# Optimization experiments

Hardware: AMD Instinct MI355X
Metric: run time of the kernel (lower is better)

The kernel has to match this reference:

```python
import jax, jax.numpy as jnp
import numpy as np

TEMPERATURE = 0.07
LOG_EPS = 1e-20
MEAN_EPS = 1e-6


def setup_inputs() -> dict:
    key = jax.random.key(0)
    k1, k2, k3 = jax.random.split(key, 3)
    B, T1, I1, C = 64, 33, 197, 512  # 1+seqlen=33, 1+14*14=197
    text_embeds = jax.random.normal(k1, (B, T1, C), dtype=jnp.float32)
    video_embeds = jax.random.normal(k2, (B, I1, C), dtype=jnp.float32)
    text_attn_mask = jax.random.randint(k3, (B, T1), 0, 2).astype(jnp.int32)
    # guarantee every row has at least one attended (non-CLS) token
    text_attn_mask = text_attn_mask.at[:, :2].set(1)
    return {"text_embeds": text_embeds, "video_embeds": video_embeds,
            "text_attn_mask": text_attn_mask}


def reference(text_embeds, video_embeds, text_attn_mask):
    # NOTE: original normalizes over dim=1 (sequence axis), kept faithfully.
    te = text_embeds / jnp.linalg.norm(text_embeds, axis=1, keepdims=True)
    ve = video_embeds / jnp.linalg.norm(video_embeds, axis=1, keepdims=True)
    mask = text_attn_mask[:, 1:].astype(bool)          # [B, T] (trim CLS)
    text_latents = te[:, 1:, :]                        # [B, T, C]
    # full late-interaction score tensor, scaled (multiplied) by temperature
    sim = jnp.einsum('xtd,yid->xyti', text_latents, ve) * TEMPERATURE  # [X,Y,T,I]

    # text -> image: max over image tokens, masked mean over text tokens
    t2i = sim.max(axis=-1)                             # [X, Y, T]
    m = mask[None, :, None, :]                         # [1, B, 1, T] (X must == B)
    numer = jnp.where(m, t2i[None], 0.0).sum(axis=-1)  # [1, B, Y]
    denom = jnp.maximum(mask.sum(axis=-1).astype(sim.dtype), MEAN_EPS)[None, :, None]
    text_to_image = numer / denom                      # [1, B, Y]

    # image -> text: masked max over text tokens, mean over image tokens
    # (computed in the original module but unused in the returned loss)
    m5 = mask[None, :, None, :, None]                  # [1, B, 1, T, 1]
    neg = -jnp.finfo(sim.dtype).max
    image_to_text = jnp.where(m5, sim[None], neg).max(axis=-2).mean(axis=-1)  # [1,B,Y]
    del image_to_text  # dead in original: loss = text_to_image_loss only

    t2i_exp = jnp.exp(text_to_image)                   # [1, B, Y]
    pos = jnp.diagonal(t2i_exp, axis1=-2, axis2=-1)    # [1, min(B, Y)]
    den = t2i_exp.sum(axis=-1)                         # [1, B]
    loss = -jnp.log(pos / den + LOG_EPS).mean(axis=-1)  # [1]
    return loss
```

## Files before the change

### kernel.cpp

```cpp
#include <hip/hip_runtime.h>
#include <hip/hip_bf16.h>
#include <float.h>
#include <math.h>

#define BB 64
#define T1 33
#define TT 32
#define II 197
#define CC 512
#define TEMP 0.07f

typedef float f32x4 __attribute__((ext_vector_type(4)));
typedef int i32x4 __attribute__((ext_vector_type(4)));
typedef int i32x8 __attribute__((ext_vector_type(8)));

#define TL_OFF  0
#define VE_OFF  (1 << 20)
#define TTI_OFF ((1 << 20) + (8 << 20))
#define KS_STRIDE   32768
#define GRP_STRIDE  131072

__global__ __launch_bounds__(512) void norm_all_kernel(const float* __restrict__ text,
                                                       const float* __restrict__ video,
                                                       unsigned char* __restrict__ tl8,
                                                       unsigned char* __restrict__ ve8) {
  int b = blockIdx.x, hz = blockIdx.y, tid = threadIdx.x;
  bool isV = hz < 4;
  int h2 = isV ? hz : hz - 4;
  const float* src = isV ? (video + (size_t)b * II * CC) : (text + (size_t)b * T1 * CC);
  int n = isV ? II : T1;

  __shared__ float cache[II][132];
  __shared__ float red[16][128];
  __shared__ float rn[128];

  {
    int c4 = tid & 31, rg = tid >> 5;
    const float* p = src + h2 * 128 + c4 * 4;
    float4 s = {0.f, 0.f, 0.f, 0.f};
    for (int i = rg; i < n; i += 16) {
      float4 v = *(const float4*)(p + (size_t)i * CC);
      *(float4*)&cache[i][c4 * 4] = v;
      s.x += v.x * v.x; s.y += v.y * v.y; s.z += v.z * v.z; s.w += v.w * v.w;
    }
    *(float4*)&red[rg][c4 * 4] = s;
  }
  __syncthreads();
  if (tid < 128) {
    float s = 0.f;
#pragma unroll
    for (int g = 0; g < 16; ++g) s += red[g][tid];
    rn[tid] = 1.0f / sqrtf(s);
  }
  __syncthreads();

  if (isV) {
    for (int S = tid; S < 13 * 128; S += 512) {
      int fb = S >> 7, h = (S >> 6) & 1, lane = S & 63;
      int i = fb * 16 + (lane & 15);
      int kloc = ((lane >> 4) & 3) * 32 + h * 16;
      unsigned int wd[4];
#pragma unroll
      for (int q = 0; q < 4; ++q) {
        f32x4 u = {0.f, 0.f, 0.f, 0.f};
        if (i < II) u = *(const f32x4*)&cache[i][kloc + q * 4];
        f32x4 r = *(const f32x4*)&rn[kloc + q * 4];
        int wv = __builtin_amdgcn_cvt_pk_fp8_f32(u[0] * r[0], u[1] * r[1], 0, 0);
        wv = __builtin_amdgcn_cvt_pk_fp8_f32(u[2] * r[2], u[3] * r[3], wv, 1);
        wd[q] = (unsigned int)wv;
      }
      unsigned char* dst = ve8 + (size_t)b * GRP_STRIDE + h2 * KS_STRIDE +
                           fb * 2048 + h * 1024 + lane * 16;
      *(uint4*)dst = make_uint4(wd[0], wd[1], wd[2], wd[3]);
    }
  } else if (tid < 256) {
    int fa_local = tid >> 7, h = (tid >> 6) & 1, lane = tid & 63;
    int t = fa_local * 16 + (lane & 15);
    int kloc = ((lane >> 4) & 3) * 32 + h * 16;
    unsigned int wd[4];
#pragma unroll
    for (int q = 0; q < 4; ++q) {
      f32x4 u = *(const f32x4*)&cache[1 + t][kloc + q * 4];
      f32x4 r = *(const f32x4*)&rn[kloc + q * 4];
      int wv = __builtin_amdgcn_cvt_pk_fp8_f32(u[0] * r[0], u[1] * r[1], 0, 0);
      wv = __builtin_amdgcn_cvt_pk_fp8_f32(u[2] * r[2], u[3] * r[3], wv, 1);
      wd[q] = (unsigned int)wv;
    }
    int fa = (b & 7) * 2 + fa_local;
    unsigned char* dst = tl8 + (size_t)(b >> 3) * GRP_STRIDE + h2 * KS_STRIDE +
                         fa * 2048 + h * 1024 + lane * 16;
    *(uint4*)dst = make_uint4(wd[0], wd[1], wd[2], wd[3]);
  }
}

__global__ __launch_bounds__(512, 4) void sim_kernel(const unsigned char* __restrict__ tl8,
                                                     const unsigned char* __restrict__ ve8,
                                                     const int* __restrict__ mask,
                                                     float* __restrict__ tti) {
  int L = blockIdx.x;
  int xcd = L & 7;
  int idx = L >> 3;
  int y = xcd * 8 + (idx & 7);
  int xcb = idx >> 3;

  int tid = threadIdx.x;
  int w = tid >> 6, lane = tid & 63;
  int wm = w & 1;
  int wn = w >> 1;

  __shared__ float smax[4 * 64];

  const unsigned char* Abase =
      tl8 + (size_t)(xcb >> 2) * GRP_STRIDE + (size_t)(xcb & 3) * 4 * 2048;
  const unsigned char* Bbase = ve8 + (size_t)y * GRP_STRIDE;

  f32x4 acc[2][4] = {};

#pragma unroll 1
  for (int s = 0; s < 4; ++s) {
    const unsigned char* ab = Abase + (size_t)s * KS_STRIDE + lane * 16;
    const unsigned char* bb = Bbase + (size_t)s * KS_STRIDE + lane * 16;

    i32x8 aop[2];
#pragma unroll
    for (int ma = 0; ma < 2; ++ma) {
      const unsigned char* p = ab + (wm * 2 + ma) * 2048;
      i32x4 h0 = *(const i32x4*)p;
      i32x4 h1 = *(const i32x4*)(p + 1024);
      aop[ma] = __builtin_shufflevector(h0, h1, 0, 1, 2, 3, 4, 5, 6, 7);
    }

#pragma unroll
    for (int nb = 0; nb < 3; ++nb) {
      int fb = wn + 4 * nb;
      const unsigned char* p = bb + fb * 2048;
      i32x4 h0 = *(const i32x4*)p;
      i32x4 h1 = *(const i32x4*)(p + 1024);
      i32x8 bop = __builtin_shufflevector(h0, h1, 0, 1, 2, 3, 4, 5, 6, 7);
#pragma unroll
      for (int ma = 0; ma < 2; ++ma)
        acc[ma][nb] = __builtin_amdgcn_mfma_scale_f32_16x16x128_f8f6f4(
            aop[ma], bop, acc[ma][nb], 0, 0,
            0, 0x7F7F7F7F, 0, 0x7F7F7F7F);
    }
    if (wn == 0) {
      const unsigned char* p = bb + 12 * 2048;
      i32x4 h0 = *(const i32x4*)p;
      i32x4 h1 = *(const i32x4*)(p + 1024);
      i32x8 bop = __builtin_shufflevector(h0, h1, 0, 1, 2, 3, 4, 5, 6, 7);
#pragma unroll
      for (int ma = 0; ma < 2; ++ma)
        acc[ma][3] = __builtin_amdgcn_mfma_scale_f32_16x16x128_f8f6f4(
            aop[ma], bop, acc[ma][3], 0, 0,
            0, 0x7F7F7F7F, 0, 0x7F7F7F7F);
    }
  }

  int col = lane & 15, gq = lane >> 4;
  int nfrag = (wn == 0) ? 4 : 3;
  bool valid[4];
#pragma unroll
  for (int nb = 0; nb < 4; ++nb) {
    int fb = wn + 4 * nb;
    valid[nb] = (nb < nfrag) && (fb * 16 + col < II);
  }

  float mx[2][4];
#pragma unroll
  for (int ma = 0; ma < 2; ++ma)
#pragma unroll
    for (int reg = 0; reg < 4; ++reg) {
      float m = -FLT_MAX;
#pragma unroll
      for (int nb = 0; nb < 4; ++nb)
        if (valid[nb]) m = fmaxf(m, acc[ma][nb][reg]);
      mx[ma][reg] = m;
    }
#pragma unroll
  for (int st = 1; st <= 8; st <<= 1)
#pragma unroll
    for (int ma = 0; ma < 2; ++ma)
#pragma unroll
      for (int reg = 0; reg < 4; ++reg)
        mx[ma][reg] = fmaxf(mx[ma][reg], __shfl_xor(mx[ma][reg], st));

  if (col == 0) {
#pragma unroll
    for (int ma = 0; ma < 2; ++ma)
#pragma unroll
      for (int reg = 0; reg < 4; ++reg)
        smax[wn * 64 + wm * 32 + ma * 16 + gq * 4 + reg] = mx[ma][reg];
  }
  __syncthreads();

  if (tid < 64) {
    int r = tid;
    float m = fmaxf(fmaxf(smax[r], smax[64 + r]),
                    fmaxf(smax[128 + r], smax[192 + r]));
    int x = xcb * 2 + (r >> 5), tt = r & 31;
    int mk = mask[x * T1 + 1 + tt];
    float num = mk ? m * TEMP : 0.f;
    float cnt = mk ? 1.f : 0.f;
#pragma unroll
    for (int st = 1; st < 32; st <<= 1) {
      num += __shfl_xor(num, st);
      cnt += __shfl_xor(cnt, st);
    }
    if (tt == 0) tti[x * 64 + y] = num / fmaxf(cnt, 1e-6f);
  }
}

__global__ void loss_kernel(const float* __restrict__ tti, float* __restrict__ out) {
  __shared__ float lxs[64];
  int tid = threadIdx.x;
  int x = tid >> 4, q = tid & 15;
  float4 v = *(const float4*)&tti[x * 64 + q * 4];
  float den = expf(v.x) + expf(v.y) + expf(v.z) + expf(v.w);
#pragma unroll
  for (int st = 1; st < 16; st <<= 1) den += __shfl_xor(den, st);
  if (q == 0) {
    float pos = expf(tti[x * 64 + x]);
    lxs[x] = -logf(pos / den + 1e-20f);
  }
  __syncthreads();
  if (tid < 64) {
    float lx = lxs[tid];
#pragma unroll
    for (int s = 1; s < 64; s <<= 1) lx += __shfl_xor(lx, s);
    if (tid == 0) out[0] = lx * (1.0f / 64.0f);
  }
}

extern "C" void kernel_launch(void* const* d_in, const int* in_sizes, int n_in,
                              void* d_out, int out_size, void* d_ws, size_t ws_size,
                              hipStream_t stream) {
  const float* text = (const float*)d_in[0];
  const float* video = (const float*)d_in[1];
  const int* mask = (const int*)d_in[2];
  float* out = (float*)d_out;

  char* ws = (char*)d_ws;
  unsigned char* tl8 = (unsigned char*)(ws + TL_OFF);
  unsigned char* ve8 = (unsigned char*)(ws + VE_OFF);
  float* tti = (float*)(ws + TTI_OFF);

  hipLaunchKernelGGL(norm_all_kernel, dim3(BB, 8), dim3(512), 0, stream, text, video, tl8, ve8);
  hipLaunchKernelGGL(sim_kernel, dim3(2048), dim3(512), 0, stream, tl8, ve8, mask, tti);
  hipLaunchKernelGGL(loss_kernel, dim3(1), dim3(1024), 0, stream, tti, out);
}
```

Baseline: 41.88 us.

## Store bf16 cache in norm kernel and software-pipeline sim kernel loads

```diff
diff --git a/kernel.cpp b/kernel.cpp
--- a/kernel.cpp
+++ b/kernel.cpp
@@ -13,6 +13,16 @@
 typedef float f32x4 __attribute__((ext_vector_type(4)));
 typedef int i32x4 __attribute__((ext_vector_type(4)));
 typedef int i32x8 __attribute__((ext_vector_type(8)));
+typedef unsigned short u16x8 __attribute__((ext_vector_type(8)));
+
+__device__ __forceinline__ unsigned short f32_to_bf16(float f) {
+  unsigned int u = __float_as_uint(f);
+  unsigned int r = u + 0x7FFFu + ((u >> 16) & 1u);
+  return (unsigned short)(r >> 16);
+}
+__device__ __forceinline__ float b2f(unsigned short u) {
+  return __uint_as_float((unsigned int)u << 16);
+}
 
 #define TL_OFF  0
 #define VE_OFF  (1 << 20)
@@ -20,17 +30,17 @@
 #define KS_STRIDE   32768
 #define GRP_STRIDE  131072
 
-__global__ __launch_bounds__(512) void norm_all_kernel(const float* __restrict__ text,
-                                                       const float* __restrict__ video,
-                                                       unsigned char* __restrict__ tl8,
-                                                       unsigned char* __restrict__ ve8) {
+__global__ __launch_bounds__(512, 4) void norm_all_kernel(const float* __restrict__ text,
+                                                          const float* __restrict__ video,
+                                                          unsigned char* __restrict__ tl8,
+                                                          unsigned char* __restrict__ ve8) {
   int b = blockIdx.x, hz = blockIdx.y, tid = threadIdx.x;
   bool isV = hz < 4;
   int h2 = isV ? hz : hz - 4;
   const float* src = isV ? (video + (size_t)b * II * CC) : (text + (size_t)b * T1 * CC);
   int n = isV ? II : T1;
 
-  __shared__ float cache[II][132];
+  __shared__ unsigned short cache[II][136];
   __shared__ float red[16][128];
   __shared__ float rn[128];
 
@@ -40,8 +50,10 @@
     float4 s = {0.f, 0.f, 0.f, 0.f};
     for (int i = rg; i < n; i += 16) {
       float4 v = *(const float4*)(p + (size_t)i * CC);
-      *(float4*)&cache[i][c4 * 4] = v;
       s.x += v.x * v.x; s.y += v.y * v.y; s.z += v.z * v.z; s.w += v.w * v.w;
+      unsigned int o0 = f32_to_bf16(v.x) | ((unsigned int)f32_to_bf16(v.y) << 16);
+      unsigned int o1 = f32_to_bf16(v.z) | ((unsigned int)f32_to_bf16(v.w) << 16);
+      *(uint2*)&cache[i][c4 * 4] = make_uint2(o0, o1);
     }
     *(float4*)&red[rg][c4 * 4] = s;
   }
@@ -59,14 +71,20 @@
       int fb = S >> 7, h = (S >> 6) & 1, lane = S & 63;
       int i = fb * 16 + (lane & 15);
       int kloc = ((lane >> 4) & 3) * 32 + h * 16;
+      u16x8 v0 = {0, 0, 0, 0, 0, 0, 0, 0}, v1 = {0, 0, 0, 0, 0, 0, 0, 0};
+      if (i < II) {
+        v0 = *(const u16x8*)&cache[i][kloc];
+        v1 = *(const u16x8*)&cache[i][kloc + 8];
+      }
+      float c[16];
+#pragma unroll
+      for (int j = 0; j < 8; ++j) { c[j] = b2f(v0[j]); c[8 + j] = b2f(v1[j]); }
       unsigned int wd[4];
 #pragma unroll
       for (int q = 0; q < 4; ++q) {
-        f32x4 u = {0.f, 0.f, 0.f, 0.f};
-        if (i < II) u = *(const f32x4*)&cache[i][kloc + q * 4];
         f32x4 r = *(const f32x4*)&rn[kloc + q * 4];
-        int wv = __builtin_amdgcn_cvt_pk_fp8_f32(u[0] * r[0], u[1] * r[1], 0, 0);
-        wv = __builtin_amdgcn_cvt_pk_fp8_f32(u[2] * r[2], u[3] * r[3], wv, 1);
+        int wv = __builtin_amdgcn_cvt_pk_fp8_f32(c[q * 4] * r[0], c[q * 4 + 1] * r[1], 0, 0);
+        wv = __builtin_amdgcn_cvt_pk_fp8_f32(c[q * 4 + 2] * r[2], c[q * 4 + 3] * r[3], wv, 1);
         wd[q] = (unsigned int)wv;
       }
       unsigned char* dst = ve8 + (size_t)b * GRP_STRIDE + h2 * KS_STRIDE +
@@ -77,13 +95,17 @@
     int fa_local = tid >> 7, h = (tid >> 6) & 1, lane = tid & 63;
     int t = fa_local * 16 + (lane & 15);
     int kloc = ((lane >> 4) & 3) * 32 + h * 16;
+    u16x8 v0 = *(const u16x8*)&cache[1 + t][kloc];
+    u16x8 v1 = *(const u16x8*)&cache[1 + t][kloc + 8];
+    float c[16];
+#pragma unroll
+    for (int j = 0; j < 8; ++j) { c[j] = b2f(v0[j]); c[8 + j] = b2f(v1[j]); }
     unsigned int wd[4];
 #pragma unroll
     for (int q = 0; q < 4; ++q) {
-      f32x4 u = *(const f32x4*)&cache[1 + t][kloc + q * 4];
       f32x4 r = *(const f32x4*)&rn[kloc + q * 4];
-      int wv = __builtin_amdgcn_cvt_pk_fp8_f32(u[0] * r[0], u[1] * r[1], 0, 0);
-      wv = __builtin_amdgcn_cvt_pk_fp8_f32(u[2] * r[2], u[3] * r[3], wv, 1);
+      int wv = __builtin_amdgcn_cvt_pk_fp8_f32(c[q * 4] * r[0], c[q * 4 + 1] * r[1], 0, 0);
+      wv = __builtin_amdgcn_cvt_pk_fp8_f32(c[q * 4 + 2] * r[2], c[q * 4 + 3] * r[3], wv, 1);
       wd[q] = (unsigned int)wv;
     }
     int fa = (b & 7) * 2 + fa_local;
@@ -110,51 +132,77 @@
 
   __shared__ float smax[4 * 64];
 
-  const unsigned char* Abase =
-      tl8 + (size_t)(xcb >> 2) * GRP_STRIDE + (size_t)(xcb & 3) * 4 * 2048;
-  const unsigned char* Bbase = ve8 + (size_t)y * GRP_STRIDE;
+  const unsigned char* Ab = tl8 + (size_t)(xcb >> 2) * GRP_STRIDE +
+                            (size_t)(xcb & 3) * 4 * 2048 +
+                            (size_t)(wm * 2) * 2048 + lane * 16;
+  const unsigned char* Bb = ve8 + (size_t)y * GRP_STRIDE +
+                            (size_t)wn * 2048 + lane * 16;
 
   f32x4 acc[2][4] = {};
 
-#pragma unroll 1
-  for (int s = 0; s < 4; ++s) {
-    const unsigned char* ab = Abase + (size_t)s * KS_STRIDE + lane * 16;
-    const unsigned char* bb = Bbase + (size_t)s * KS_STRIDE + lane * 16;
-
-    i32x8 aop[2];
-#pragma unroll
-    for (int ma = 0; ma < 2; ++ma) {
-      const unsigned char* p = ab + (wm * 2 + ma) * 2048;
-      i32x4 h0 = *(const i32x4*)p;
-      i32x4 h1 = *(const i32x4*)(p + 1024);
-      aop[ma] = __builtin_shufflevector(h0, h1, 0, 1, 2, 3, 4, 5, 6, 7);
-    }
-
-#pragma unroll
-    for (int nb = 0; nb < 3; ++nb) {
-      int fb = wn + 4 * nb;
-      const unsigned char* p = bb + fb * 2048;
-      i32x4 h0 = *(const i32x4*)p;
-      i32x4 h1 = *(const i32x4*)(p + 1024);
-      i32x8 bop = __builtin_shufflevector(h0, h1, 0, 1, 2, 3, 4, 5, 6, 7);
-#pragma unroll
-      for (int ma = 0; ma < 2; ++ma)
-        acc[ma][nb] = __builtin_amdgcn_mfma_scale_f32_16x16x128_f8f6f4(
-            aop[ma], bop, acc[ma][nb], 0, 0,
-            0, 0x7F7F7F7F, 0, 0x7F7F7F7F);
-    }
-    if (wn == 0) {
-      const unsigned char* p = bb + 12 * 2048;
-      i32x4 h0 = *(const i32x4*)p;
-      i32x4 h1 = *(const i32x4*)(p + 1024);
-      i32x8 bop = __builtin_shufflevector(h0, h1, 0, 1, 2, 3, 4, 5, 6, 7);
-#pragma unroll
-      for (int ma = 0; ma < 2; ++ma)
-        acc[ma][3] = __builtin_amdgcn_mfma_scale_f32_16x16x128_f8f6f4(
-            aop[ma], bop, acc[ma][3], 0, 0,
-            0, 0x7F7F7F7F, 0, 0x7F7F7F7F);
-    }
-  }
+#define MFMA_(aop, bop, c) __builtin_amdgcn_mfma_scale_f32_16x16x128_f8f6f4( \
+      aop, bop, c, 0, 0, 0, 0x7F7F7F7F, 0, 0x7F7F7F7F)
+#define SHUF_(a, b) __builtin_shufflevector(a, b, 0, 1, 2, 3, 4, 5, 6, 7)
+
+#define LDA_(d0, d1, d2, d3, s_) do {                                         \
+    const unsigned char* p_ = Ab + (size_t)(s_) * KS_STRIDE;                  \
+    d0 = *(const i32x4*)p_;          d1 = *(const i32x4*)(p_ + 1024);         \
+    d2 = *(const i32x4*)(p_ + 2048); d3 = *(const i32x4*)(p_ + 3072);         \
+  } while (0)
+#define LDB_(d0, d1, s_) do {                                                 \
+    const unsigned char* p_ = Bb + (size_t)(s_) * KS_STRIDE;                  \
+    d0 = *(const i32x4*)p_; d1 = *(const i32x4*)(p_ + 1024);                  \
+  } while (0)
+
+#define COMP_(s_, a0, a1, a2, a3, b0, b1) do {                                \
+    i32x8 aop0_ = SHUF_(a0, a1), aop1_ = SHUF_(a2, a3);                       \
+    i32x8 bop_ = SHUF_(b0, b1);                                               \
+    acc[0][0] = MFMA_(aop0_, bop_, acc[0][0]);                                \
+    acc[1][0] = MFMA_(aop1_, bop_, acc[1][0]);                                \
+    {                                                                         \
+      const unsigned char* p_ = Bb + (size_t)(s_) * KS_STRIDE + 8192;         \
+      i32x4 t0_ = *(const i32x4*)p_, t1_ = *(const i32x4*)(p_ + 1024);        \
+      bop_ = SHUF_(t0_, t1_);                                                 \
+      acc[0][1] = MFMA_(aop0_, bop_, acc[0][1]);                              \
+      acc[1][1] = MFMA_(aop1_, bop_, acc[1][1]);                              \
+    }                                                                         \
+    {                                                                         \
+      const unsigned char* p_ = Bb + (size_t)(s_) * KS_STRIDE + 16384;        \
+      i32x4 t0_ = *(const i32x4*)p_, t1_ = *(const i32x4*)(p_ + 1024);        \
+      bop_ = SHUF_(t0_, t1_);                                                 \
+      acc[0][2] = MFMA_(aop0_, bop_, acc[0][2]);                              \
+      acc[1][2] = MFMA_(aop1_, bop_, acc[1][2]);                              \
+    }                                                                         \
+    if (wn == 0) {                                                            \
+      const unsigned char* p_ = Bb + (size_t)(s_) * KS_STRIDE + 24576;        \
+      i32x4 t0_ = *(const i32x4*)p_, t1_ = *(const i32x4*)(p_ + 1024);        \
+      bop_ = SHUF_(t0_, t1_);                                                 \
+      acc[0][3] = MFMA_(aop0_, bop_, acc[0][3]);                              \
+      acc[1][3] = MFMA_(aop1_, bop_, acc[1][3]);                              \
+    }                                                                         \
+  } while (0)
+
+  i32x4 cA0, cA1, cA2, cA3, nA0, nA1, nA2, nA3;
+  i32x4 cB0, cB1, nB0, nB1;
+
+  LDA_(cA0, cA1, cA2, cA3, 0); LDB_(cB0, cB1, 0);
+  LDA_(nA0, nA1, nA2, nA3, 1); LDB_(nB0, nB1, 1);
+
+  COMP_(0, cA0, cA1, cA2, cA3, cB0, cB1);
+  asm volatile("" ::: "memory");
+  LDA_(cA0, cA1, cA2, cA3, 2); LDB_(cB0, cB1, 2);
+  COMP_(1, nA0, nA1, nA2, nA3, nB0, nB1);
+  asm volatile("" ::: "memory");
+  LDA_(nA0, nA1, nA2, nA3, 3); LDB_(nB0, nB1, 3);
+  COMP_(2, cA0, cA1, cA2, cA3, cB0, cB1);
+  asm volatile("" ::: "memory");
+  COMP_(3, nA0, nA1, nA2, nA3, nB0, nB1);
+
+#undef LDA_
+#undef LDB_
+#undef COMP_
+#undef MFMA_
+#undef SHUF_
 
   int col = lane & 15, gq = lane >> 4;
   int nfrag = (wn == 0) ? 4 : 3;
```

After: 42.61 us. No clear change (+1.8%).
